# Kernel tuning notes

Hardware: AMD Instinct MI355X
Metric: run time of the kernel (lower is better)

The kernel has to match this reference:

```python
import jax, jax.numpy as jnp
import numpy as np

DIM = 128
SCALE = (DIM // 8) ** -0.5  # head_dim**-0.5 with default num_heads=8 (heads never actually split)


def _attention(x, fm, qw, kw, vw, pw, pb):
    # x, fm: [B, C, H, W]
    B, C, H, W = x.shape
    xt = x.reshape(B, C, H * W).transpose(0, 2, 1)   # [B, N, C]
    ft = fm.reshape(B, C, H * W).transpose(0, 2, 1)  # [B, N, C]
    q = jnp.einsum('bnc,dc->bnd', xt, qw)
    k = jnp.einsum('bnc,dc->bnd', ft, kw)
    v = jnp.einsum('bnc,dc->bnd', xt, vw)
    attn = jax.nn.softmax(jnp.einsum('bnd,bmd->bnm', q, k) * SCALE, axis=-1)
    o = jnp.einsum('bnm,bmd->bnd', attn, v)
    o = jnp.einsum('bnd,ed->bne', o, pw) + pb
    return o.transpose(0, 2, 1).reshape(B, C, H, W)


def setup_inputs() -> dict:
    key = jax.random.key(0)
    ks = jax.random.split(key, 16)
    B, C, H, W = 1, DIM, 96, 96
    s = 0.02
    inp = {
        'x': jax.random.normal(ks[0], (B, C, H, W), jnp.float32),
        'featuremap': jax.random.normal(ks[1], (B, C, H, W), jnp.float32),
        'hm': jax.random.uniform(ks[2], (B, 1, H, W), jnp.float32),
        'obj_qw': jax.random.normal(ks[3], (C, C), jnp.float32) * s,
        'obj_kw': jax.random.normal(ks[4], (C, C), jnp.float32) * s,
        'obj_vw': jax.random.normal(ks[5], (C, C), jnp.float32) * s,
        'obj_pw': jax.random.normal(ks[6], (C, C), jnp.float32) * s,
        'obj_pb': jnp.zeros((C,), jnp.float32),
        'bg_qw': jax.random.normal(ks[7], (C, C), jnp.float32) * s,
        'bg_kw': jax.random.normal(ks[8], (C, C), jnp.float32) * s,
        'bg_vw': jax.random.normal(ks[9], (C, C), jnp.float32) * s,
        'bg_pw': jax.random.normal(ks[10], (C, C), jnp.float32) * s,
        'bg_pb': jnp.zeros((C,), jnp.float32),
        'conv_w': jax.random.normal(ks[11], (C, C, 3, 3), jnp.float32) * s,
        'conv_b': jnp.zeros((C,), jnp.float32),
    }
    return inp


def reference(x, featuremap, hm, obj_qw, obj_kw, obj_vw, obj_pw, obj_pb,
              bg_qw, bg_kw, bg_vw, bg_pw, bg_pb, conv_w, conv_b):
    obj_mask = jnp.where(hm > 0.3, 1.0, 0.01)
    bg_mask = jnp.where(hm <= 0.3, 1.0, 0.01)
    obj_att = _attention(x * obj_mask, featuremap * obj_mask,
                         obj_qw, obj_kw, obj_vw, obj_pw, obj_pb)
    bg_att = _attention(x * bg_mask, featuremap * bg_mask,
                        bg_qw, bg_kw, bg_vw, bg_pw, bg_pb)
    am = obj_att + bg_att
    out = jax.lax.conv_general_dilated(
        am, conv_w, window_strides=(1, 1), padding='SAME',
        dimension_numbers=('NCHW', 'OIHW', 'NCHW'))
    return out + conv_b[None, :, None, None]
```

## Files before the change

kernel.cpp:

```cpp
#include <hip/hip_runtime.h>


typedef unsigned short u16;
typedef short bf16x8 __attribute__((ext_vector_type(8)));
typedef float f32x4 __attribute__((ext_vector_type(4)));

#define MFMA(a, b, c) __builtin_amdgcn_mfma_f32_16x16x32_bf16((a), (b), (c), 0, 0, 0)

#define NN 9216
#define CC 128

__device__ __forceinline__ u16 f2b(float f) {
  union { float f; unsigned int u; } v; v.f = f;
  unsigned int u = v.u + 0x7fffu + ((v.u >> 16) & 1u);
  return (u16)(u >> 16);
}

__device__ __forceinline__ unsigned int f2b2(float lo, float hi) {
  return (unsigned int)f2b(lo) | ((unsigned int)f2b(hi) << 16);
}

__device__ __forceinline__ unsigned int pkhi(float a, float b) {
  return __builtin_amdgcn_perm(__float_as_uint(b), __float_as_uint(a), 0x07060302u);
}

__device__ __forceinline__ bf16x8 ldb(const u16* p) { return *(const bf16x8*)p; }

__global__ void k_transpose(const float* __restrict__ x, const float* __restrict__ fm,
                            u16* __restrict__ xt, u16* __restrict__ fmt) {
  __shared__ float tile[32][33];
  const float* src = blockIdx.z ? fm : x;
  u16* dst = blockIdx.z ? fmt : xt;
  int n0 = blockIdx.x * 32, c0 = blockIdx.y * 32;
  int tx = threadIdx.x & 31, ty = threadIdx.x >> 5;
#pragma unroll
  for (int i = 0; i < 4; i++)
    tile[ty + i * 8][tx] = src[(c0 + ty + i * 8) * NN + n0 + tx];
  __syncthreads();
#pragma unroll
  for (int i = 0; i < 4; i++)
    dst[(n0 + ty + i * 8) * CC + c0 + tx] = f2b(tile[tx][ty + i * 8]);
}

__global__ void k_cvtw(const float* s0, const float* s1, const float* s2, const float* s3,
                       const float* s4, const float* s5, const float* s6, const float* s7,
                       u16* __restrict__ dst) {
  const float* arr[8] = {s0, s1, s2, s3, s4, s5, s6, s7};
  int a = blockIdx.y;
  int i = blockIdx.x * 256 + threadIdx.x;
  dst[a * 16384 + i] = f2b(arr[a][i]);
}

__global__ void k_cvtconv(const float* __restrict__ cw, u16* __restrict__ wp) {
  int i = blockIdx.x * 256 + threadIdx.x;
  int khkw = i >> 14; int rem = i & 16383; int o = rem >> 7; int ii = rem & 127;
  wp[i] = f2b(cw[(o * 128 + ii) * 9 + khkw]);
}

__global__ __launch_bounds__(256) void k_qkv(
    const u16* __restrict__ xt, const u16* __restrict__ fmt, const float* __restrict__ hm,
    const u16* __restrict__ wall, u16* __restrict__ Q, u16* __restrict__ K,
    u16* __restrict__ Vt) {
  int wid = threadIdx.x >> 6, lane = threadIdx.x & 63;
  int quad = lane >> 4, c = lane & 15;
  int nt = blockIdx.x * 4 + wid;
  int arr = blockIdx.y;
  int attn = arr / 3, kind = arr % 3;
  int nb = nt * 16;
  const u16* A = (kind == 1) ? fmt : xt;
  const u16* W = wall + (attn * 4 + kind) * 16384;

  if (kind < 2) {
    bf16x8 af[4];
#pragma unroll
    for (int ks = 0; ks < 4; ks++)
      af[ks] = ldb(A + (nb + c) * CC + ks * 32 + quad * 8);
    float msk[4];
#pragma unroll
    for (int r = 0; r < 4; r++) {
      bool obj = hm[nb + quad * 4 + r] > 0.3f;
      float mv = (attn == 0) ? (obj ? 1.f : 0.01f) : (obj ? 0.01f : 1.f);
      msk[r] = (kind == 0) ? mv * 0.3606737602222409f : mv;
    }
    u16* out = (kind == 0 ? Q : K) + attn * NN * CC;
#pragma unroll
    for (int dt = 0; dt < 8; dt++) {
      f32x4 acc = {0.f, 0.f, 0.f, 0.f};
#pragma unroll
      for (int ks = 0; ks < 4; ks++)
        acc = MFMA(af[ks], ldb(W + (dt * 16 + c) * CC + ks * 32 + quad * 8), acc);
#pragma unroll
      for (int r = 0; r < 4; r++)
        out[(nb + quad * 4 + r) * CC + dt * 16 + c] = f2b(acc[r] * msk[r]);
    }
  } else {
    bf16x8 bfr[4];
#pragma unroll
    for (int ks = 0; ks < 4; ks++)
      bfr[ks] = ldb(A + (nb + c) * CC + ks * 32 + quad * 8);
    bool obj = hm[nb + c] > 0.3f;
    float mv = (attn == 0) ? (obj ? 1.f : 0.01f) : (obj ? 0.01f : 1.f);
    u16* out = Vt + attn * CC * NN;
#pragma unroll
    for (int dt = 0; dt < 8; dt++) {
      f32x4 acc = {0.f, 0.f, 0.f, 0.f};
#pragma unroll
      for (int ks = 0; ks < 4; ks++)
        acc = MFMA(ldb(W + (dt * 16 + c) * CC + ks * 32 + quad * 8), bfr[ks], acc);
#pragma unroll
      for (int r = 0; r < 4; r++)
        out[(dt * 16 + quad * 4 + r) * NN + nb + c] = f2b(acc[r] * mv);
    }
  }
}

#define FITERS 36
#define KLDS 8704
#define VLDS 10240
__global__ __launch_bounds__(256, 2) void k_flash(
    const u16* __restrict__ Q, const u16* __restrict__ K, const u16* __restrict__ Vt,
    u16* __restrict__ U, float* __restrict__ L) {
  __shared__ __align__(16) char lds[48128];
  int tid = threadIdx.x;
  int wid = tid >> 6, lane = tid & 63;
  int quad = lane >> 4, c = lane & 15;
  int b = blockIdx.x;
  int qg = b >> 4; int combo = b & 15;
  int attn = combo >> 3; int ks = combo & 7;
  int nb = qg * 128 + wid * 32;
  const u16* q = Q + attn * NN * CC;
  const u16* kg = K + attn * NN * CC;
  const u16* vg = Vt + attn * CC * NN;
  int kb0 = ks * 1152;

  int krow = tid >> 4, kch = tid & 15;
  const u16* gkp0 = kg + (kb0 + krow) * CC + kch * 8;
  const u16* gkp1 = gkp0 + 16 * CC;
  int lk0 = krow * 272 + kch * 16, lk1 = lk0 + 16 * 272;
  int vrow = tid >> 2, vqd = tid & 3;
  const u16* gvp0 = vg + vrow * NN + kb0 + vqd * 8;
  const u16* gvp1 = gvp0 + 64 * NN;
  int lv0 = vrow * 80 + vqd * 16, lv1 = lv0 + 64 * 80;

  bf16x8 qf[2][4];
#pragma unroll
  for (int qt = 0; qt < 2; qt++)
#pragma unroll
    for (int k4 = 0; k4 < 4; k4++)
      qf[qt][k4] = ldb(q + (nb + qt * 16 + c) * CC + k4 * 32 + quad * 8);

  const bf16x8 ONES = {(short)0x3F80, (short)0x3F80, (short)0x3F80, (short)0x3F80,
                       (short)0x3F80, (short)0x3F80, (short)0x3F80, (short)0x3F80};

  f32x4 O[2][8];
  f32x4 lacc[2];
#pragma unroll
  for (int qt = 0; qt < 2; qt++) {
#pragma unroll
    for (int dt = 0; dt < 8; dt++) O[qt][dt] = (f32x4){0.f, 0.f, 0.f, 0.f};
    lacc[qt] = (f32x4){0.f, 0.f, 0.f, 0.f};
  }

  char* Pw = lds + 37888 + wid * 2560;

  uint4 gk0 = *(const uint4*)gkp0, gk1 = *(const uint4*)gkp1;
  uint4 gv0 = *(const uint4*)gvp0, gv1 = *(const uint4*)gvp1;

  for (int it = 0; it < FITERS; it++) {
    char* kb_lds = lds + ((it & 1) ? KLDS : 0);
    char* vb_lds = lds + 17408 + ((it & 1) ? VLDS : 0);
    *(uint4*)(kb_lds + lk0) = gk0;
    *(uint4*)(kb_lds + lk1) = gk1;
    *(uint4*)(vb_lds + lv0) = gv0;
    *(uint4*)(vb_lds + lv1) = gv1;
    if (it + 1 < FITERS) {
      gkp0 += 32 * CC; gkp1 += 32 * CC; gvp0 += 32; gvp1 += 32;
      gk0 = *(const uint4*)gkp0; gk1 = *(const uint4*)gkp1;
      gv0 = *(const uint4*)gvp0; gv1 = *(const uint4*)gvp1;
    }
    __syncthreads();

    bf16x8 kf[2][4];
#pragma unroll
    for (int kt = 0; kt < 2; kt++)
#pragma unroll
      for (int k4 = 0; k4 < 4; k4++)
        kf[kt][k4] = *(const bf16x8*)(kb_lds + (kt * 16 + c) * 272 + k4 * 64 + quad * 16);

#pragma unroll
    for (int qt = 0; qt < 2; qt++) {
      f32x4 s0 = {0.f, 0.f, 0.f, 0.f}, s1 = {0.f, 0.f, 0.f, 0.f};
#pragma unroll
      for (int k4 = 0; k4 < 4; k4++) {
        s0 = MFMA(kf[0][k4], qf[qt][k4], s0);
        s1 = MFMA(kf[1][k4], qf[qt][k4], s1);
      }
      uint2 d0, d1;
      d0.x = pkhi(__builtin_amdgcn_exp2f(s0[0]), __builtin_amdgcn_exp2f(s0[1]));
      d0.y = pkhi(__builtin_amdgcn_exp2f(s0[2]), __builtin_amdgcn_exp2f(s0[3]));
      d1.x = pkhi(__builtin_amdgcn_exp2f(s1[0]), __builtin_amdgcn_exp2f(s1[1]));
      d1.y = pkhi(__builtin_amdgcn_exp2f(s1[2]), __builtin_amdgcn_exp2f(s1[3]));
      char* prow = Pw + (qt * 16 + c) * 80;
      *(uint2*)(prow + quad * 8) = d0;
      *(uint2*)(prow + 32 + quad * 8) = d1;
    }

    bf16x8 vf[8];
#pragma unroll
    for (int dt = 0; dt < 8; dt++)
      vf[dt] = *(const bf16x8*)(vb_lds + (dt * 16 + c) * 80 + quad * 16);

#pragma unroll
    for (int qt = 0; qt < 2; qt++) {
      bf16x8 pf = *(const bf16x8*)(Pw + (qt * 16 + c) * 80 + quad * 16);
      lacc[qt] = MFMA(pf, ONES, lacc[qt]);
#pragma unroll
      for (int dt = 0; dt < 8; dt++) O[qt][dt] = MFMA(pf, vf[dt], O[qt][dt]);
    }
  }

  int p = attn * 8 + ks;
  u16* up = U + (p * NN + nb) * CC;
#pragma unroll
  for (int qt = 0; qt < 2; qt++)
#pragma unroll
    for (int dt = 0; dt < 8; dt++)
#pragma unroll
      for (int r = 0; r < 4; r++)
        up[(qt * 16 + quad * 4 + r) * CC + dt * 16 + c] = f2b(O[qt][dt][r]);
  if (c == 0) {
#pragma unroll
    for (int qt = 0; qt < 2; qt++)
#pragma unroll
      for (int r = 0; r < 4; r++)
        L[p * NN + nb + qt * 16 + quad * 4 + r] = lacc[qt][r];
  }
}

__global__ void k_merge(const u16* __restrict__ U, const float* __restrict__ L,
                        u16* __restrict__ Om) {
  int t = blockIdx.x * 256 + threadIdx.x;
  int attn = t / (NN * 32); int rem = t % (NN * 32);
  int n = rem >> 5; int d4 = (rem & 31) * 4;
  float a0 = 0.f, a1 = 0.f, a2 = 0.f, a3 = 0.f, l = 0.f;
#pragma unroll
  for (int s = 0; s < 8; s++) {
    int p = attn * 8 + s;
    uint2 u = *(const uint2*)(U + (p * NN + n) * CC + d4);
    a0 += __uint_as_float(u.x << 16);
    a1 += __uint_as_float(u.x & 0xffff0000u);
    a2 += __uint_as_float(u.y << 16);
    a3 += __uint_as_float(u.y & 0xffff0000u);
    l += L[p * NN + n];
  }
  float inv = 1.f / l;
  uint2 pk;
  pk.x = f2b2(a0 * inv, a1 * inv);
  pk.y = f2b2(a2 * inv, a3 * inv);
  *(uint2*)(Om + ((long)attn * NN + n) * CC + d4) = pk;
}

__global__ __launch_bounds__(256) void k_proj(const u16* __restrict__ Om,
                                              const u16* __restrict__ wall,
                                              const float* __restrict__ pb0,
                                              const float* __restrict__ pb1,
                                              u16* __restrict__ amt) {
  int wid = threadIdx.x >> 6, lane = threadIdx.x & 63;
  int quad = lane >> 4, c = lane & 15;
  int nb = blockIdx.x * 16;
  bf16x8 af[2][4];
#pragma unroll
  for (int a = 0; a < 2; a++)
#pragma unroll
    for (int k4 = 0; k4 < 4; k4++)
      af[a][k4] = ldb(Om + ((long)a * NN + nb + c) * CC + k4 * 32 + quad * 8);
  const u16* wpo = wall + 3 * 16384;
  const u16* wpb = wall + 7 * 16384;
#pragma unroll
  for (int eh = 0; eh < 2; eh++) {
    int et = wid * 2 + eh;
    f32x4 acc = {0.f, 0.f, 0.f, 0.f};
#pragma unroll
    for (int k4 = 0; k4 < 4; k4++)
      acc = MFMA(af[0][k4], ldb(wpo + (et * 16 + c) * CC + k4 * 32 + quad * 8), acc);
#pragma unroll
    for (int k4 = 0; k4 < 4; k4++)
      acc = MFMA(af[1][k4], ldb(wpb + (et * 16 + c) * CC + k4 * 32 + quad * 8), acc);
    float bias = pb0[et * 16 + c] + pb1[et * 16 + c];
#pragma unroll
    for (int r = 0; r < 4; r++)
      amt[(nb + quad * 4 + r) * CC + et * 16 + c] = f2b(acc[r] + bias);
  }
}

__global__ __launch_bounds__(256) void k_conv(const u16* __restrict__ amt,
                                              const u16* __restrict__ wp,
                                              const float* __restrict__ cb,
                                              float* __restrict__ out) {
  int wid = threadIdx.x >> 6, lane = threadIdx.x & 63;
  int quad = lane >> 4, c = lane & 15;
  int p = blockIdx.x * 16 + c;
  int h = p / 96, w = p % 96;
  f32x4 acc[2];
  acc[0] = (f32x4){0.f, 0.f, 0.f, 0.f};
  acc[1] = (f32x4){0.f, 0.f, 0.f, 0.f};
  const bf16x8 zv = {0, 0, 0, 0, 0, 0, 0, 0};
#pragma unroll
  for (int kh = 0; kh < 3; kh++)
#pragma unroll
    for (int kw = 0; kw < 3; kw++) {
      int hh = h + kh - 1, ww = w + kw - 1;
      bool valid = (hh >= 0) && (hh < 96) && (ww >= 0) && (ww < 96);
      int sp = hh * 96 + ww;
      const u16* wbase = wp + (kh * 3 + kw) * 16384;
#pragma unroll
      for (int k4 = 0; k4 < 4; k4++) {
        bf16x8 bv = zv;
        if (valid) bv = ldb(amt + sp * CC + k4 * 32 + quad * 8);
#pragma unroll
        for (int oi = 0; oi < 2; oi++) {
          int ot = wid * 2 + oi;
          acc[oi] = MFMA(ldb(wbase + (ot * 16 + c) * CC + k4 * 32 + quad * 8), bv, acc[oi]);
        }
      }
    }
#pragma unroll
  for (int oi = 0; oi < 2; oi++)
#pragma unroll
    for (int r = 0; r < 4; r++) {
      int o = (wid * 2 + oi) * 16 + quad * 4 + r;
      out[o * NN + p] = acc[oi][r] + cb[o];
    }
}

extern "C" void kernel_launch(void* const* d_in, const int* in_sizes, int n_in,
                              void* d_out, int out_size, void* d_ws, size_t ws_size,
                              hipStream_t stream) {
  (void)in_sizes; (void)n_in; (void)out_size; (void)ws_size;
  const float* x   = (const float*)d_in[0];
  const float* fm  = (const float*)d_in[1];
  const float* hm  = (const float*)d_in[2];
  const float* qw0 = (const float*)d_in[3];
  const float* kw0 = (const float*)d_in[4];
  const float* vw0 = (const float*)d_in[5];
  const float* pw0 = (const float*)d_in[6];
  const float* pb0 = (const float*)d_in[7];
  const float* qw1 = (const float*)d_in[8];
  const float* kw1 = (const float*)d_in[9];
  const float* vw1 = (const float*)d_in[10];
  const float* pw1 = (const float*)d_in[11];
  const float* pb1 = (const float*)d_in[12];
  const float* cw  = (const float*)d_in[13];
  const float* cb  = (const float*)d_in[14];
  float* out = (float*)d_out;
  char* ws = (char*)d_ws;

  u16*   XT   = (u16*)(ws + 0);
  u16*   FMT  = (u16*)(ws + 2359296);
  u16*   WALL = (u16*)(ws + 4718592);
  u16*   WCV  = (u16*)(ws + 4980736);
  u16*   QQ   = (u16*)(ws + 5275648);
  u16*   KK   = (u16*)(ws + 9994240);
  u16*   VT   = (u16*)(ws + 14712832);
  u16*   UU   = (u16*)(ws + 19431424);
  float* LL   = (float*)(ws + 57180160);
  u16*   OM   = QQ;
  u16*   AMT  = KK;

  k_transpose<<<dim3(288, 4, 2), 256, 0, stream>>>(x, fm, XT, FMT);
  k_cvtw<<<dim3(64, 8), 256, 0, stream>>>(qw0, kw0, vw0, pw0, qw1, kw1, vw1, pw1, WALL);
  k_cvtconv<<<576, 256, 0, stream>>>(cw, WCV);
  k_qkv<<<dim3(144, 6), 256, 0, stream>>>(XT, FMT, hm, WALL, QQ, KK, VT);
  k_flash<<<1152, 256, 0, stream>>>(QQ, KK, VT, UU, LL);
  k_merge<<<2304, 256, 0, stream>>>(UU, LL, OM);
  k_proj<<<576, 256, 0, stream>>>(OM, WALL, pb0, pb1, AMT);
  k_conv<<<576, 256, 0, stream>>>(AMT, WCV, cb, out);
}
```

Measured before the change: 270.3 us.

## Enlarge flash query tile, make split count adaptive, fuse merge into projection

Each flash wave now handles 64 query rows instead of 32, so every K/V tile loaded into LDS is reused across twice as many queries. The key-split count rises from 8 to 16 when the workspace is large enough. The split-merge kernel is fused into the output projection through an LDS staging buffer, and the three prep kernels are merged into one launch. The larger tile raises register pressure and could lower occupancy, while more splits add partial-result traffic that the fused merge has to read.

```diff
diff --git a/kernel.cpp b/kernel.cpp
--- a/kernel.cpp
+++ b/kernel.cpp
@@ -26,35 +26,39 @@
 
 __device__ __forceinline__ bf16x8 ldb(const u16* p) { return *(const bf16x8*)p; }
 
-__global__ void k_transpose(const float* __restrict__ x, const float* __restrict__ fm,
-                            u16* __restrict__ xt, u16* __restrict__ fmt) {
-  __shared__ float tile[32][33];
-  const float* src = blockIdx.z ? fm : x;
-  u16* dst = blockIdx.z ? fmt : xt;
-  int n0 = blockIdx.x * 32, c0 = blockIdx.y * 32;
-  int tx = threadIdx.x & 31, ty = threadIdx.x >> 5;
-#pragma unroll
-  for (int i = 0; i < 4; i++)
-    tile[ty + i * 8][tx] = src[(c0 + ty + i * 8) * NN + n0 + tx];
-  __syncthreads();
-#pragma unroll
-  for (int i = 0; i < 4; i++)
-    dst[(n0 + ty + i * 8) * CC + c0 + tx] = f2b(tile[tx][ty + i * 8]);
-}
-
-__global__ void k_cvtw(const float* s0, const float* s1, const float* s2, const float* s3,
-                       const float* s4, const float* s5, const float* s6, const float* s7,
-                       u16* __restrict__ dst) {
-  const float* arr[8] = {s0, s1, s2, s3, s4, s5, s6, s7};
-  int a = blockIdx.y;
-  int i = blockIdx.x * 256 + threadIdx.x;
-  dst[a * 16384 + i] = f2b(arr[a][i]);
-}
-
-__global__ void k_cvtconv(const float* __restrict__ cw, u16* __restrict__ wp) {
-  int i = blockIdx.x * 256 + threadIdx.x;
-  int khkw = i >> 14; int rem = i & 16383; int o = rem >> 7; int ii = rem & 127;
-  wp[i] = f2b(cw[(o * 128 + ii) * 9 + khkw]);
+__global__ void k_prep(const float* __restrict__ x, const float* __restrict__ fm,
+                       const float* qw0, const float* kw0, const float* vw0,
+                       const float* pw0, const float* qw1, const float* kw1,
+                       const float* vw1, const float* pw1,
+                       const float* __restrict__ cw,
+                       u16* __restrict__ xt, u16* __restrict__ fmt,
+                       u16* __restrict__ wall, u16* __restrict__ wp) {
+  int bid = blockIdx.x, tid = threadIdx.x;
+  if (bid < 2304) {
+    __shared__ float tile[32][33];
+    int z = bid / 1152, b2 = bid % 1152;
+    const float* src = z ? fm : x;
+    u16* dst = z ? fmt : xt;
+    int n0 = (b2 % 288) * 32, c0 = (b2 / 288) * 32;
+    int tx = tid & 31, ty = tid >> 5;
+#pragma unroll
+    for (int i = 0; i < 4; i++)
+      tile[ty + i * 8][tx] = src[(c0 + ty + i * 8) * NN + n0 + tx];
+    __syncthreads();
+#pragma unroll
+    for (int i = 0; i < 4; i++)
+      dst[(n0 + ty + i * 8) * CC + c0 + tx] = f2b(tile[tx][ty + i * 8]);
+  } else if (bid < 2816) {
+    const float* arr[8] = {qw0, kw0, vw0, pw0, qw1, kw1, vw1, pw1};
+    int b2 = bid - 2304;
+    int a = b2 >> 6;
+    int i = (b2 & 63) * 256 + tid;
+    wall[a * 16384 + i] = f2b(arr[a][i]);
+  } else {
+    int i = (bid - 2816) * 256 + tid;
+    int khkw = i >> 14; int rem = i & 16383; int o = rem >> 7; int ii = rem & 127;
+    wp[i] = f2b(cw[(o * 128 + ii) * 9 + khkw]);
+  }
 }
 
 __global__ __launch_bounds__(256) void k_qkv(
@@ -114,24 +118,21 @@
   }
 }
 
-#define FITERS 36
-#define KLDS 8704
-#define VLDS 10240
 __global__ __launch_bounds__(256, 2) void k_flash(
     const u16* __restrict__ Q, const u16* __restrict__ K, const u16* __restrict__ Vt,
-    u16* __restrict__ U, float* __restrict__ L) {
-  __shared__ __align__(16) char lds[48128];
+    u16* __restrict__ U, float* __restrict__ L, int S, int niters) {
+  __shared__ __align__(16) char lds[58368];
   int tid = threadIdx.x;
   int wid = tid >> 6, lane = tid & 63;
   int quad = lane >> 4, c = lane & 15;
   int b = blockIdx.x;
-  int qg = b >> 4; int combo = b & 15;
-  int attn = combo >> 3; int ks = combo & 7;
-  int nb = qg * 128 + wid * 32;
+  int qg = b / (2 * S); int combo = b % (2 * S);
+  int attn = combo / S; int ks = combo % S;
+  int nb = qg * 256 + wid * 64;
   const u16* q = Q + attn * NN * CC;
   const u16* kg = K + attn * NN * CC;
   const u16* vg = Vt + attn * CC * NN;
-  int kb0 = ks * 1152;
+  int kb0 = ks * (NN / S);
 
   int krow = tid >> 4, kch = tid & 15;
   const u16* gkp0 = kg + (kb0 + krow) * CC + kch * 8;
@@ -142,9 +143,9 @@
   const u16* gvp1 = gvp0 + 64 * NN;
   int lv0 = vrow * 80 + vqd * 16, lv1 = lv0 + 64 * 80;
 
-  bf16x8 qf[2][4];
-#pragma unroll
-  for (int qt = 0; qt < 2; qt++)
+  bf16x8 qf[4][4];
+#pragma unroll
+  for (int qt = 0; qt < 4; qt++)
 #pragma unroll
     for (int k4 = 0; k4 < 4; k4++)
       qf[qt][k4] = ldb(q + (nb + qt * 16 + c) * CC + k4 * 32 + quad * 8);
@@ -152,77 +153,70 @@
   const bf16x8 ONES = {(short)0x3F80, (short)0x3F80, (short)0x3F80, (short)0x3F80,
                        (short)0x3F80, (short)0x3F80, (short)0x3F80, (short)0x3F80};
 
-  f32x4 O[2][8];
-  f32x4 lacc[2];
-#pragma unroll
-  for (int qt = 0; qt < 2; qt++) {
+  f32x4 O[4][8];
+  f32x4 lacc[4];
+#pragma unroll
+  for (int qt = 0; qt < 4; qt++) {
 #pragma unroll
     for (int dt = 0; dt < 8; dt++) O[qt][dt] = (f32x4){0.f, 0.f, 0.f, 0.f};
     lacc[qt] = (f32x4){0.f, 0.f, 0.f, 0.f};
   }
 
-  char* Pw = lds + 37888 + wid * 2560;
+  char* Pw = lds + 37888 + wid * 5120;
 
   uint4 gk0 = *(const uint4*)gkp0, gk1 = *(const uint4*)gkp1;
   uint4 gv0 = *(const uint4*)gvp0, gv1 = *(const uint4*)gvp1;
 
-  for (int it = 0; it < FITERS; it++) {
-    char* kb_lds = lds + ((it & 1) ? KLDS : 0);
-    char* vb_lds = lds + 17408 + ((it & 1) ? VLDS : 0);
+  for (int it = 0; it < niters; it++) {
+    char* kb_lds = lds + ((it & 1) ? 8704 : 0);
+    char* vb_lds = lds + 17408 + ((it & 1) ? 10240 : 0);
     *(uint4*)(kb_lds + lk0) = gk0;
     *(uint4*)(kb_lds + lk1) = gk1;
     *(uint4*)(vb_lds + lv0) = gv0;
     *(uint4*)(vb_lds + lv1) = gv1;
-    if (it + 1 < FITERS) {
+    if (it + 1 < niters) {
       gkp0 += 32 * CC; gkp1 += 32 * CC; gvp0 += 32; gvp1 += 32;
       gk0 = *(const uint4*)gkp0; gk1 = *(const uint4*)gkp1;
       gv0 = *(const uint4*)gvp0; gv1 = *(const uint4*)gvp1;
     }
     __syncthreads();
 
-    bf16x8 kf[2][4];
-#pragma unroll
-    for (int kt = 0; kt < 2; kt++)
+#pragma unroll
+    for (int kt = 0; kt < 2; kt++) {
+      bf16x8 kf[4];
 #pragma unroll
       for (int k4 = 0; k4 < 4; k4++)
-        kf[kt][k4] = *(const bf16x8*)(kb_lds + (kt * 16 + c) * 272 + k4 * 64 + quad * 16);
-
-#pragma unroll
-    for (int qt = 0; qt < 2; qt++) {
-      f32x4 s0 = {0.f, 0.f, 0.f, 0.f}, s1 = {0.f, 0.f, 0.f, 0.f};
-#pragma unroll
-      for (int k4 = 0; k4 < 4; k4++) {
-        s0 = MFMA(kf[0][k4], qf[qt][k4], s0);
-        s1 = MFMA(kf[1][k4], qf[qt][k4], s1);
+        kf[k4] = *(const bf16x8*)(kb_lds + (kt * 16 + c) * 272 + k4 * 64 + quad * 16);
+#pragma unroll
+      for (int qt = 0; qt < 4; qt++) {
+        f32x4 s = {0.f, 0.f, 0.f, 0.f};
+#pragma unroll
+        for (int k4 = 0; k4 < 4; k4++) s = MFMA(kf[k4], qf[qt][k4], s);
+        uint2 d;
+        d.x = pkhi(__builtin_amdgcn_exp2f(s[0]), __builtin_amdgcn_exp2f(s[1]));
+        d.y = pkhi(__builtin_amdgcn_exp2f(s[2]), __builtin_amdgcn_exp2f(s[3]));
+        *(uint2*)(Pw + (qt * 16 + c) * 80 + kt * 32 + quad * 8) = d;
       }
-      uint2 d0, d1;
-      d0.x = pkhi(__builtin_amdgcn_exp2f(s0[0]), __builtin_amdgcn_exp2f(s0[1]));
-      d0.y = pkhi(__builtin_amdgcn_exp2f(s0[2]), __builtin_amdgcn_exp2f(s0[3]));
-      d1.x = pkhi(__builtin_amdgcn_exp2f(s1[0]), __builtin_amdgcn_exp2f(s1[1]));
-      d1.y = pkhi(__builtin_amdgcn_exp2f(s1[2]), __builtin_amdgcn_exp2f(s1[3]));
-      char* prow = Pw + (qt * 16 + c) * 80;
-      *(uint2*)(prow + quad * 8) = d0;
-      *(uint2*)(prow + 32 + quad * 8) = d1;
-    }
-
-    bf16x8 vf[8];
-#pragma unroll
-    for (int dt = 0; dt < 8; dt++)
-      vf[dt] = *(const bf16x8*)(vb_lds + (dt * 16 + c) * 80 + quad * 16);
-
-#pragma unroll
-    for (int qt = 0; qt < 2; qt++) {
-      bf16x8 pf = *(const bf16x8*)(Pw + (qt * 16 + c) * 80 + quad * 16);
-      lacc[qt] = MFMA(pf, ONES, lacc[qt]);
-#pragma unroll
-      for (int dt = 0; dt < 8; dt++) O[qt][dt] = MFMA(pf, vf[dt], O[qt][dt]);
-    }
-  }
-
-  int p = attn * 8 + ks;
-  u16* up = U + (p * NN + nb) * CC;
-#pragma unroll
-  for (int qt = 0; qt < 2; qt++)
+    }
+
+    bf16x8 pf[4];
+#pragma unroll
+    for (int qt = 0; qt < 4; qt++) {
+      pf[qt] = *(const bf16x8*)(Pw + (qt * 16 + c) * 80 + quad * 16);
+      lacc[qt] = MFMA(pf[qt], ONES, lacc[qt]);
+    }
+#pragma unroll
+    for (int dt = 0; dt < 8; dt++) {
+      bf16x8 vf = *(const bf16x8*)(vb_lds + (dt * 16 + c) * 80 + quad * 16);
+#pragma unroll
+      for (int qt = 0; qt < 4; qt++) O[qt][dt] = MFMA(pf[qt], vf, O[qt][dt]);
+    }
+  }
+
+  int p = attn * S + ks;
+  u16* up = U + (long)(p * NN + nb) * CC;
+#pragma unroll
+  for (int qt = 0; qt < 4; qt++)
 #pragma unroll
     for (int dt = 0; dt < 8; dt++)
 #pragma unroll
@@ -230,50 +224,69 @@
         up[(qt * 16 + quad * 4 + r) * CC + dt * 16 + c] = f2b(O[qt][dt][r]);
   if (c == 0) {
 #pragma unroll
-    for (int qt = 0; qt < 2; qt++)
+    for (int qt = 0; qt < 4; qt++)
 #pragma unroll
       for (int r = 0; r < 4; r++)
         L[p * NN + nb + qt * 16 + quad * 4 + r] = lacc[qt][r];
   }
 }
 
-__global__ void k_merge(const u16* __restrict__ U, const float* __restrict__ L,
-                        u16* __restrict__ Om) {
-  int t = blockIdx.x * 256 + threadIdx.x;
-  int attn = t / (NN * 32); int rem = t % (NN * 32);
-  int n = rem >> 5; int d4 = (rem & 31) * 4;
-  float a0 = 0.f, a1 = 0.f, a2 = 0.f, a3 = 0.f, l = 0.f;
-#pragma unroll
-  for (int s = 0; s < 8; s++) {
-    int p = attn * 8 + s;
-    uint2 u = *(const uint2*)(U + (p * NN + n) * CC + d4);
-    a0 += __uint_as_float(u.x << 16);
-    a1 += __uint_as_float(u.x & 0xffff0000u);
-    a2 += __uint_as_float(u.y << 16);
-    a3 += __uint_as_float(u.y & 0xffff0000u);
-    l += L[p * NN + n];
-  }
-  float inv = 1.f / l;
-  uint2 pk;
-  pk.x = f2b2(a0 * inv, a1 * inv);
-  pk.y = f2b2(a2 * inv, a3 * inv);
-  *(uint2*)(Om + ((long)attn * NN + n) * CC + d4) = pk;
-}
-
-__global__ __launch_bounds__(256) void k_proj(const u16* __restrict__ Om,
-                                              const u16* __restrict__ wall,
-                                              const float* __restrict__ pb0,
-                                              const float* __restrict__ pb1,
-                                              u16* __restrict__ amt) {
-  int wid = threadIdx.x >> 6, lane = threadIdx.x & 63;
+__global__ __launch_bounds__(256) void k_pm(const u16* __restrict__ U,
+                                            const float* __restrict__ L,
+                                            const u16* __restrict__ wall,
+                                            const float* __restrict__ pb0,
+                                            const float* __restrict__ pb1,
+                                            u16* __restrict__ amt, int S) {
+  __shared__ __align__(16) char omt[8704];
+  __shared__ float linv[32];
+  int tid = threadIdx.x;
+  int nb = blockIdx.x * 16;
+
+  {
+    if (tid < 32) {
+      int a = tid >> 4, r = tid & 15;
+      float l = 0.f;
+      for (int s = 0; s < S; s++) l += L[(a * S + s) * NN + nb + r];
+      linv[tid] = 1.f / l;
+    }
+    int a = tid >> 7, rr = (tid >> 3) & 15, dg = tid & 7;
+    float acc[16];
+#pragma unroll
+    for (int j = 0; j < 16; j++) acc[j] = 0.f;
+    for (int s = 0; s < S; s++) {
+      const u16* src = U + (long)((a * S + s) * NN + nb + rr) * CC + dg * 16;
+      uint4 u0 = *(const uint4*)src;
+      uint4 u1 = *(const uint4*)(src + 8);
+      const unsigned int* w0 = (const unsigned int*)&u0;
+      const unsigned int* w1 = (const unsigned int*)&u1;
+#pragma unroll
+      for (int j = 0; j < 4; j++) {
+        acc[j * 2 + 0] += __uint_as_float(w0[j] << 16);
+        acc[j * 2 + 1] += __uint_as_float(w0[j] & 0xffff0000u);
+        acc[8 + j * 2 + 0] += __uint_as_float(w1[j] << 16);
+        acc[8 + j * 2 + 1] += __uint_as_float(w1[j] & 0xffff0000u);
+      }
+    }
+    __syncthreads();
+    float inv = linv[a * 16 + rr];
+    unsigned int pk[8];
+#pragma unroll
+    for (int j = 0; j < 8; j++)
+      pk[j] = f2b2(acc[j * 2] * inv, acc[j * 2 + 1] * inv);
+    uint4* dst = (uint4*)(omt + (a * 16 + rr) * 272 + dg * 32);
+    dst[0] = *(uint4*)&pk[0];
+    dst[1] = *(uint4*)&pk[4];
+  }
+  __syncthreads();
+
+  int wid = tid >> 6, lane = tid & 63;
   int quad = lane >> 4, c = lane & 15;
-  int nb = blockIdx.x * 16;
   bf16x8 af[2][4];
 #pragma unroll
   for (int a = 0; a < 2; a++)
 #pragma unroll
     for (int k4 = 0; k4 < 4; k4++)
-      af[a][k4] = ldb(Om + ((long)a * NN + nb + c) * CC + k4 * 32 + quad * 8);
+      af[a][k4] = *(const bf16x8*)(omt + (a * 16 + c) * 272 + k4 * 64 + quad * 16);
   const u16* wpo = wall + 3 * 16384;
   const u16* wpb = wall + 7 * 16384;
 #pragma unroll
@@ -336,7 +349,7 @@
 extern "C" void kernel_launch(void* const* d_in, const int* in_sizes, int n_in,
                               void* d_out, int out_size, void* d_ws, size_t ws_size,
                               hipStream_t stream) {
-  (void)in_sizes; (void)n_in; (void)out_size; (void)ws_size;
+  (void)in_sizes; (void)n_in; (void)out_size;
   const float* x   = (const float*)d_in[0];
   const float* fm  = (const float*)d_in[1];
   const float* hm  = (const float*)d_in[2];
@@ -355,6 +368,9 @@
   float* out = (float*)d_out;
   char* ws = (char*)d_ws;
 
+  int S = (ws_size >= 96200000u) ? 16 : 8;
+  int niters = (NN / S) / 32;
+
   u16*   XT   = (u16*)(ws + 0);
   u16*   FMT  = (u16*)(ws + 2359296);
   u16*   WALL = (u16*)(ws + 4718592);
@@ -363,16 +379,13 @@
   u16*   KK   = (u16*)(ws + 9994240);
   u16*   VT   = (u16*)(ws + 14712832);
   u16*   UU   = (u16*)(ws + 19431424);
-  float* LL   = (float*)(ws + 57180160);
-  u16*   OM   = QQ;
+  float* LL   = (float*)(ws + 19431424 + (size_t)2 * S * NN * CC * 2);
   u16*   AMT  = KK;
 
-  k_transpose<<<dim3(288, 4, 2), 256, 0, stream>>>(x, fm, XT, FMT);
-  k_cvtw<<<dim3(64, 8), 256, 0, stream>>>(qw0, kw0, vw0, pw0, qw1, kw1, vw1, pw1, WALL);
-  k_cvtconv<<<576, 256, 0, stream>>>(cw, WCV);
+  k_prep<<<3392, 256, 0, stream>>>(x, fm, qw0, kw0, vw0, pw0, qw1, kw1, vw1, pw1,
+                                   cw, XT, FMT, WALL, WCV);
   k_qkv<<<dim3(144, 6), 256, 0, stream>>>(XT, FMT, hm, WALL, QQ, KK, VT);
-  k_flash<<<1152, 256, 0, stream>>>(QQ, KK, VT, UU, LL);
-  k_merge<<<2304, 256, 0, stream>>>(UU, LL, OM);
-  k_proj<<<576, 256, 0, stream>>>(OM, WALL, pb0, pb1, AMT);
+  k_flash<<<36 * 2 * S, 256, 0, stream>>>(QQ, KK, VT, UU, LL, S, niters);
+  k_pm<<<576, 256, 0, stream>>>(UU, LL, WALL, pb0, pb1, AMT, S);
   k_conv<<<576, 256, 0, stream>>>(AMT, WCV, cb, out);
 }
```

Result: slower. 277.7 us (+2.7%).
